# Optimization experiments

Hardware: AMD Instinct MI355X
Metric: run time of the kernel (lower is better)

## Reference

```python
import jax, jax.numpy as jnp
import numpy as np

B, N = 8, 2048          # clouds x points per cloud
M1, M2 = 1024, 256      # centroids after ratio 0.5, then 0.25
K = 64                  # max_num_neighbors
R1, R2 = 0.2, 0.4       # radii
CURV_K = 10             # knn for curvature
CURV_SCALAR = 10.0      # Net(curvature_scalar)
NEG = -1e30


def _sqdist(a, b):
    # squared pairwise distances [len(a), len(b)] without an [.,.,3] intermediate
    return jnp.sum(a * a, -1)[:, None] + jnp.sum(b * b, -1)[None, :] - 2.0 * (a @ b.T)


def _mlp3(x, Wa, ba, Wb, bb, Wc, bc):
    # torch_geometric MLP: Linear+ReLU hidden layers, plain last layer
    h = jax.nn.relu(x @ Wa + ba)
    h = jax.nn.relu(h @ Wb + bb)
    return h @ Wc + bc


def _curvature(pos):
    # per-point surface variation lambda_min / sum(lambda) over k-NN covariance
    d2 = _sqdist(pos, pos)                        # [N,N]
    _, idx = jax.lax.top_k(-d2, CURV_K)           # k nearest (incl. self)
    nbr = pos[idx]                                # [N,k,3]
    c = nbr - jnp.mean(nbr, 1, keepdims=True)
    cov = jnp.einsum('nki,nkj->nij', c, c) / CURV_K
    ev = jnp.linalg.eigvalsh(cov)                 # ascending
    return ev[:, 0] / (jnp.sum(ev, -1) + 1e-8)


def _fps_weighted(pos, curv, m):
    # farthest point sampling, min-distance score weighted by curvature
    w = 1.0 + CURV_SCALAR * curv
    d0 = jnp.sum((pos - pos[0]) ** 2, -1)
    def step(min_d2, _):
        i = jnp.argmax(min_d2 * w)
        nd = jnp.sum((pos - pos[i]) ** 2, -1)
        return jnp.minimum(min_d2, nd), i
    _, rest = jax.lax.scan(step, d0, None, length=m - 1)
    return jnp.concatenate([jnp.zeros((1,), rest.dtype), rest])


def _sa(x, pos, curv, m, r, params):
    # SAModule: weighted FPS -> radius grouping (cap K) -> PointNetConv (gather, MLP, max)
    idx = _fps_weighted(pos, curv, m)
    cpos = pos[idx]                               # [m,3]
    d2 = _sqdist(cpos, pos)                       # [m,N]
    score = jnp.where(d2 <= r * r, -d2, NEG)
    vals, nidx = jax.lax.top_k(score, K)          # up to K nearest within radius
    mask = vals > NEG * 0.5                       # [m,K]
    rel = pos[nidx] - cpos[:, None, :]            # [m,K,3]
    feats = rel if x is None else jnp.concatenate([x[nidx], rel], -1)
    msg = _mlp3(feats, *params)                   # [m,K,F]
    msg = jnp.where(mask[:, :, None], msg, NEG)
    out = jnp.max(msg, 1)                         # scatter-max aggregation
    out = jnp.where(jnp.any(mask, 1)[:, None], out, 0.0)  # empty groups -> 0
    return out, cpos, curv[idx]


def _forward(pos, W1a, b1a, W1b, b1b, W1c, b1c, W2a, b2a, W2b, b2b, W2c, b2c,
             W3a, b3a, W3b, b3b, W3c, b3c, Wh1, bh1, Wh2, bh2, Wh3, bh3):
    p1 = (W1a, b1a, W1b, b1b, W1c, b1c)
    p2 = (W2a, b2a, W2b, b2b, W2c, b2c)
    p3 = (W3a, b3a, W3b, b3b, W3c, b3c)
    def cloud(p):
        curv = _curvature(p)
        x1, pos1, c1 = _sa(None, p, curv, M1, R1, p1)
        x2, pos2, _ = _sa(x1, pos1, c1, M2, R2, p2)
        g = _mlp3(jnp.concatenate([x2, pos2], -1), *p3)   # [M2,1024]
        return jnp.max(g, 0)                              # global max pool
    gfeat = jax.vmap(cloud)(pos.reshape(B, N, 3))          # [B,1024]
    logits = _mlp3(gfeat, Wh1, bh1, Wh2, bh2, Wh3, bh3)    # dropout (eval) = id
    return jax.nn.log_softmax(logits, -1)


_LAYERS = [("W1a", "b1a", 3, 64), ("W1b", "b1b", 64, 64), ("W1c", "b1c", 64, 128),
           ("W2a", "b2a", 131, 128), ("W2b", "b2b", 128, 128), ("W2c", "b2c", 128, 256),
           ("W3a", "b3a", 259, 256), ("W3b", "b3b", 256, 512), ("W3c", "b3c", 512, 1024),
           ("Wh1", "bh1", 1024, 512), ("Wh2", "bh2", 512, 256), ("Wh3", "bh3", 256, 10)]


def setup_inputs() -> dict:
    key = jax.random.key(0)
    ks = iter(jax.random.split(key, 2 * len(_LAYERS) + 1))
    inp = {"pos": jax.random.uniform(next(ks), (B * N, 3), jnp.float32)}
    for wn, bn, fi, fo in _LAYERS:
        inp[wn] = jax.random.normal(next(ks), (fi, fo), jnp.float32) / np.sqrt(fi)
        inp[bn] = jnp.zeros((fo,), jnp.float32)
    return inp


def reference(pos, W1a, b1a, W1b, b1b, W1c, b1c, W2a, b2a, W2b, b2b, W2c, b2c,
              W3a, b3a, W3b, b3b, W3c, b3c, Wh1, bh1, Wh2, bh2, Wh3, bh3):
    return _forward(pos, W1a, b1a, W1b, b1b, W1c, b1c, W2a, b2a, W2b, b2b, W2c, b2c,
                    W3a, b3a, W3b, b3b, W3c, b3c, Wh1, bh1, Wh2, bh2, Wh3, bh3)
```

## Files before the change

### kernel.cpp

```cpp
#include <hip/hip_runtime.h>
#include <hip/hip_fp16.h>
#include <math.h>

#define TID threadIdx.x

typedef _Float16 h2vec __attribute__((ext_vector_type(2)));
typedef _Float16 f16x8 __attribute__((ext_vector_type(8)));
typedef float f32x4 __attribute__((ext_vector_type(4)));
typedef float f32x2v __attribute__((ext_vector_type(2)));

#if __has_builtin(__builtin_elementwise_fma)
#define EFMA(a, b, c) __builtin_elementwise_fma((a), (b), (c))
#else
static __device__ __forceinline__ f32x2v EFMA(f32x2v a, f32x2v b, f32x2v c) {
    f32x2v r;
    r.x = fmaf(a.x, b.x, c.x);
    r.y = fmaf(a.y, b.y, c.y);
    return r;
}
#endif

static __device__ __forceinline__ float fdot2(unsigned a, unsigned b, float c) {
    h2vec av, bv;
    __builtin_memcpy(&av, &a, 4);
    __builtin_memcpy(&bv, &b, 4);
    return __builtin_amdgcn_fdot2(av, bv, c, false);
}

static __device__ __forceinline__ unsigned packh2(float a, float b) {
    __half2 hh = __floats2half2_rn(a, b);
    unsigned u;
    __builtin_memcpy(&u, &hh, 4);
    return u;
}

static __device__ __forceinline__ unsigned encf(float f) {
    unsigned u = __float_as_uint(f);
    return (u >> 31) ? ~u : (u | 0x80000000u);
}
static __device__ __forceinline__ float decf(unsigned e) {
    unsigned u = (e >> 31) ? (e & 0x7fffffffu) : ~e;
    return __uint_as_float(u);
}

static __device__ __forceinline__ int wave_sum(int v) {
    v += __builtin_amdgcn_update_dpp(0, v, 0x111, 0xf, 0xf, true);
    v += __builtin_amdgcn_update_dpp(0, v, 0x112, 0xf, 0xf, true);
    v += __builtin_amdgcn_update_dpp(0, v, 0x114, 0xf, 0xf, true);
    v += __builtin_amdgcn_update_dpp(0, v, 0x118, 0xf, 0xf, true);
    v += __builtin_amdgcn_update_dpp(0, v, 0x142, 0xf, 0xf, true);
    v += __builtin_amdgcn_update_dpp(0, v, 0x143, 0xf, 0xf, true);
    return __builtin_amdgcn_readlane(v, 63);
}

template <int CTRL>
static __device__ __forceinline__ unsigned long long dpp_max_u64(unsigned long long k) {
    int lo = (int)(unsigned)(k & 0xffffffffULL);
    int hi = (int)(unsigned)(k >> 32);
    int lo2 = __builtin_amdgcn_update_dpp(0, lo, CTRL, 0xf, 0xf, true);
    int hi2 = __builtin_amdgcn_update_dpp(0, hi, CTRL, 0xf, 0xf, true);
    unsigned long long k2 = ((unsigned long long)(unsigned)hi2 << 32) | (unsigned)lo2;
    return k2 > k ? k2 : k;
}

static __device__ __forceinline__ void pack_slot(const float* __restrict__ W,
                                                 unsigned* __restrict__ out,
                                                 int K, int ncols, int t) {
    int lane = t & 63;
    int frag = t >> 6;
    int nct = ncols >> 4;
    int ks = frag / nct, ct = frag - ks * nct;
    int kbase = (ks << 5) + ((lane >> 4) << 3);
    int cc = (ct << 4) + (lane & 15);
    unsigned o[4];
#pragma unroll
    for (int i = 0; i < 4; ++i) {
        int k0 = kbase + 2 * i, k1 = kbase + 2 * i + 1;
        float f0 = (k0 < K) ? W[(size_t)k0 * ncols + cc] : 0.f;
        float f1 = (k1 < K) ? W[(size_t)k1 * ncols + cc] : 0.f;
        o[i] = packh2(f0, f1);
    }
    *(uint4*)&out[(size_t)t * 4] = make_uint4(o[0], o[1], o[2], o[3]);
}

__global__ __launch_bounds__(256) void curv_kernel(const float* __restrict__ pos,
                                                   float* __restrict__ curv) {
    __shared__ float4 sp[2048];
    __shared__ float smd[64][40];
    __shared__ int smi[64][40];
    int cloud = blockIdx.x >> 5;
    int base = cloud << 11;
    for (int j = TID; j < 2048; j += 256) {
        const float* p = pos + (size_t)(base + j) * 3;
        float x = p[0], y = p[1], z = p[2];
        sp[j] = make_float4(x, y, z, fmaf(x, x, fmaf(y, y, z * z)));
    }
    __syncthreads();
    int pt = TID >> 2;
    int sub = TID & 3;
    int li = ((blockIdx.x & 31) << 6) + pt;
    float4 pi = sp[li];
    float bd[10];
    int bi[10];
#pragma unroll
    for (int t = 0; t < 10; ++t) { bd[t] = 3.0e38f; bi[t] = 0; }
    int j0 = sub << 9;
    for (int jj = 0; jj < 512; ++jj) {
        int j = j0 + jj;
        float4 pj = sp[j];
        float dot = fmaf(pi.x, pj.x, fmaf(pi.y, pj.y, pi.z * pj.z));
        float d2 = pi.w + pj.w - 2.0f * dot;
        if (d2 < bd[9]) {
            bd[9] = d2; bi[9] = j;
#pragma unroll
            for (int t = 9; t > 0; --t) {
                if (bd[t] < bd[t - 1]) {
                    float td = bd[t]; bd[t] = bd[t - 1]; bd[t - 1] = td;
                    int ti = bi[t]; bi[t] = bi[t - 1]; bi[t - 1] = ti;
                }
            }
        }
    }
#pragma unroll
    for (int t = 0; t < 10; ++t) {
        smd[pt][sub * 10 + t] = bd[t];
        smi[pt][sub * 10 + t] = bi[t];
    }
    __syncthreads();
    float d0 = smd[pt][0], d1 = smd[pt][10], d2h = smd[pt][20], d3 = smd[pt][30];
    int i0 = smi[pt][0], i1 = smi[pt][10], i2 = smi[pt][20], i3 = smi[pt][30];
    int h0 = 0, h1 = 0, h2c = 0, h3 = 0;
    int mbi[10];
#pragma unroll
    for (int t = 0; t < 10; ++t) {
        bool a01 = (d1 < d0) || (d1 == d0 && i1 < i0);
        float dA = a01 ? d1 : d0; int iA = a01 ? i1 : i0;
        bool a23 = (d3 < d2h) || (d3 == d2h && i3 < i2);
        float dB = a23 ? d3 : d2h; int iB = a23 ? i3 : i2;
        bool ab = (dB < dA) || (dB == dA && iB < iA);
        mbi[t] = ab ? iB : iA;
        if (ab) {
            if (a23) { ++h3; d3 = (h3 < 10) ? smd[pt][30 + h3] : 3.0e38f;
                       i3 = (h3 < 10) ? smi[pt][30 + h3] : 0x7fffffff; }
            else     { ++h2c; d2h = (h2c < 10) ? smd[pt][20 + h2c] : 3.0e38f;
                       i2 = (h2c < 10) ? smi[pt][20 + h2c] : 0x7fffffff; }
        } else {
            if (a01) { ++h1; d1 = (h1 < 10) ? smd[pt][10 + h1] : 3.0e38f;
                       i1 = (h1 < 10) ? smi[pt][10 + h1] : 0x7fffffff; }
            else     { ++h0; d0 = (h0 < 10) ? smd[pt][h0] : 3.0e38f;
                       i0 = (h0 < 10) ? smi[pt][h0] : 0x7fffffff; }
        }
    }
    if (sub != 0) return;
    double sx = 0, sy = 0, sz = 0;
#pragma unroll
    for (int t = 0; t < 10; ++t) { float4 p = sp[mbi[t]]; sx += p.x; sy += p.y; sz += p.z; }
    double mx = sx / 10.0, my = sy / 10.0, mz = sz / 10.0;
    double cxx = 0, cxy = 0, cxz = 0, cyy = 0, cyz = 0, czz = 0;
#pragma unroll
    for (int t = 0; t < 10; ++t) {
        float4 p = sp[mbi[t]];
        double dx = p.x - mx, dy = p.y - my, dz = p.z - mz;
        cxx += dx * dx; cxy += dx * dy; cxz += dx * dz;
        cyy += dy * dy; cyz += dy * dz; czz += dz * dz;
    }
    cxx /= 10.0; cxy /= 10.0; cxz /= 10.0; cyy /= 10.0; cyz /= 10.0; czz /= 10.0;
    double q = (cxx + cyy + czz) / 3.0;
    double b00 = cxx - q, b11 = cyy - q, b22 = czz - q;
    double p2 = b00 * b00 + b11 * b11 + b22 * b22 +
                2.0 * (cxy * cxy + cxz * cxz + cyz * cyz);
    double lmin;
    if (p2 <= 0.0) {
        lmin = q;
    } else {
        double p = sqrt(p2 / 6.0);
        double inv = 1.0 / p;
        double c00 = b00 * inv, c01 = cxy * inv, c02 = cxz * inv;
        double c11 = b11 * inv, c12 = cyz * inv, c22 = b22 * inv;
        double detB = c00 * (c11 * c22 - c12 * c12)
                    - c01 * (c01 * c22 - c12 * c02)
                    + c02 * (c01 * c12 - c11 * c02);
        double r = 0.5 * detB;
        r = fmin(1.0, fmax(-1.0, r));
        double phi = acos(r) / 3.0;
        lmin = q + 2.0 * p * cos(phi + 2.0943951023931953);
    }
    double s3 = cxx + cyy + czz;
    curv[base + li] = (float)(lmin / (s3 + 1e-8));
}

template <int N, int M, int SLOTS>
static __device__ void fps_body(
    const float* __restrict__ srcpos, int stride, const float* __restrict__ srccurv,
    int cloud, float4* __restrict__ outPos, float* __restrict__ outCurv,
    float* __restrict__ outA, int ldA,
    float4* sp, int* sidx, unsigned long long* rec ) {
    constexpr int PAIRS = SLOTS / 2;
    const float* cp = srcpos + (size_t)cloud * N * stride;
    for (int j = TID; j < N; j += 256)
        sp[j] = make_float4(cp[j * stride], cp[j * stride + 1], cp[j * stride + 2], 0.f);
    if (TID == 0) sidx[0] = 0;
    __syncthreads();
    f32x2v px[PAIRS], py[PAIRS], pz[PAIRS], md[PAIRS], wvv[PAIRS];
#pragma unroll
    for (int s = 0; s < PAIRS; ++s) {
        int p0 = ((2 * s) << 8) + TID, p1 = ((2 * s + 1) << 8) + TID;
        float4 q0 = sp[p0], q1 = sp[p1];
        px[s].x = q0.x; px[s].y = q1.x;
        py[s].x = q0.y; py[s].y = q1.y;
        pz[s].x = q0.z; pz[s].y = q1.z;
        md[s].x = 3.0e38f; md[s].y = 3.0e38f;
        wvv[s].x = fmaf(10.0f, srccurv[cloud * N + p0], 1.0f);
        wvv[s].y = fmaf(10.0f, srccurv[cloud * N + p1], 1.0f);
    }
    int lane = TID & 63, w4 = TID >> 6;
    float4 c0 = sp[0];
    float cx = c0.x, cy = c0.y, cz = c0.z;
    for (int t = 1; t < M; ++t) {
        f32x2v cxv, cyv, czv;
        cxv.x = cx; cxv.y = cx; cyv.x = cy; cyv.y = cy; czv.x = cz; czv.y = cz;
        unsigned long long kk[PAIRS];
#pragma unroll
        for (int s = 0; s < PAIRS; ++s) {
            f32x2v dx = px[s] - cxv, dy = py[s] - cyv, dz = pz[s] - czv;
            f32x2v nd = EFMA(dx, dx, EFMA(dy, dy, dz * dz));
            f32x2v m2 = __builtin_elementwise_min(md[s], nd);
            md[s] = m2;
            f32x2v sc = m2 * wvv[s];
            unsigned long long k0 =
                ((unsigned long long)__float_as_uint(sc.x) << 32) |
                (unsigned)(2047 - (((2 * s) << 8) + TID));
            unsigned long long k1 =
                ((unsigned long long)__float_as_uint(sc.y) << 32) |
                (unsigned)(2047 - (((2 * s + 1) << 8) + TID));
            kk[s] = k0 > k1 ? k0 : k1;
        }
        unsigned long long k = kk[0];
#pragma unroll
        for (int s = 1; s < PAIRS; ++s) k = kk[s] > k ? kk[s] : k;
        k = dpp_max_u64<0x111>(k);
        k = dpp_max_u64<0x112>(k);
        k = dpp_max_u64<0x114>(k);
        k = dpp_max_u64<0x118>(k);
        k = dpp_max_u64<0x142>(k);
        k = dpp_max_u64<0x143>(k);
        int pbase = (t & 1) << 2;
        if (lane == 63) rec[pbase | w4] = k;
        __syncthreads();
        unsigned long long k0 = rec[pbase + 0];
        unsigned long long k1 = rec[pbase + 1];
        unsigned long long k2 = rec[pbase + 2];
        unsigned long long k3 = rec[pbase + 3];
        unsigned long long ka = k0 > k1 ? k0 : k1;
        unsigned long long kb = k2 > k3 ? k2 : k3;
        unsigned long long km = ka > kb ? ka : kb;
        int nbix = 2047 - (int)(unsigned)(km & 0xffffffffULL);
        if (TID == 0) sidx[t] = nbix;
        float4 cc = sp[nbix];
        cx = cc.x; cy = cc.y; cz = cc.z;
    }
    __syncthreads();
    for (int j = TID; j < M; j += 256) {
        int id = sidx[j];
        float4 qv = sp[id];
        outPos[cloud * M + j] = qv;
        if (outCurv) outCurv[cloud * M + j] = srccurv[cloud * N + id];
        if (outA) {
            float* a = outA + (size_t)(cloud * M + j) * ldA;
            a[256] = qv.x; a[257] = qv.y; a[258] = qv.z;
        }
    }
}

__global__ __launch_bounds__(256, 1) void fps1_pack_kernel(
    const float* __restrict__ pos, const float* __restrict__ curv,
    float4* __restrict__ pos1, float* __restrict__ curv1,
    const float* __restrict__ Wc, const float* __restrict__ Wa,
    const float* __restrict__ Wb, const float* __restrict__ W3a,
    const float* __restrict__ W3b, const float* __restrict__ W3c,
    unsigned* __restrict__ WcH, unsigned* __restrict__ WaH,
    unsigned* __restrict__ WbH, unsigned* __restrict__ W3aH,
    unsigned* __restrict__ W3bH, unsigned* __restrict__ W3cH,
    unsigned* __restrict__ gfeatE) {
    __shared__ float4 sp[2048];
    __shared__ int sidx[1024];
    __shared__ unsigned long long rec[8];
    if (blockIdx.x < 8) {
        fps_body<2048, 1024, 8>(pos, 3, curv, blockIdx.x, pos1, curv1, nullptr, 0,
                                sp, sidx, rec);
        return;
    }
    int b = blockIdx.x - 8;
    if (b == 0)
        for (int i = TID; i < 8192; i += 256) gfeatE[i] = 0u;
    if (b < 16)        pack_slot(Wc,  WcH,  128, 256,  b * 256 + TID);
    else if (b < 26)   pack_slot(Wa,  WaH,  131, 128,  (b - 16) * 256 + TID);
    else if (b < 34)   pack_slot(Wb,  WbH,  128, 128,  (b - 26) * 256 + TID);
    else if (b < 70)   pack_slot(W3a, W3aH, 259, 256,  (b - 34) * 256 + TID);
    else if (b < 134)  pack_slot(W3b, W3bH, 256, 512,  (b - 70) * 256 + TID);
    else               pack_slot(W3c, W3cH, 512, 1024, (b - 134) * 256 + TID);
}

static __device__ __forceinline__ int select_k64(const unsigned int* ck, const int* ci,
                                                 int c, int lane, int* cnt2, int* sel,
                                                 int* nbOut) {
    if (c <= 64) {
        *nbOut = c;
        return (lane < c) ? ci[lane] : 0;
    }
    unsigned int T = 0;
    for (int bit = 31; bit >= 0; --bit) {
        unsigned int mid = T | (1u << bit);
        int cl = 0;
        for (int q = lane; q < c; q += 64) cl += (ck[q] < mid) ? 1 : 0;
        if (wave_sum(cl) < 64) T = mid;
    }
    int cl = 0;
    for (int q = lane; q < c; q += 64) cl += (ck[q] < T) ? 1 : 0;
    int need = 64 - wave_sum(cl);
    int TI = 0;
    for (int bit = 11; bit >= 0; --bit) {
        int mid = TI | (1 << bit);
        int ce = 0;
        for (int q = lane; q < c; q += 64) ce += (ck[q] == T && ci[q] < mid) ? 1 : 0;
        if (wave_sum(ce) < need) TI = mid;
    }
    for (int q = lane; q < c; q += 64) {
        unsigned int kq = ck[q];
        int iq = ci[q];
        if (kq < T || (kq == T && iq <= TI)) sel[atomicAdd(cnt2, 1)] = iq;
    }
    *nbOut = 64;
    return sel[lane];
}

union U1 {
    struct {
        float4 sp[2048];
        unsigned ck[4][256];
        int ci[4][256];
        int sel[4][64];
        int cnt[4], cnt2[4];
    } p;
    unsigned h2s[4][2048];
};

static __device__ void conv1_body(
    int bid, U1& u,
    const float* __restrict__ pos, const float4* __restrict__ pos1,
    const float* __restrict__ W1, const float* __restrict__ B1,
    const float* __restrict__ W2, const float* __restrict__ B2,
    const float* __restrict__ W3, const float* __restrict__ B3,
    float* __restrict__ x1) {
    __shared__ int nbs[4];
    int cloud = bid >> 8;
    int w4 = TID >> 6, lane = TID & 63;
    int centb = (bid & 255) << 2;
    int g = (cloud << 10) + centb + w4;
    int base = cloud << 11;
    for (int j = TID; j < 2048; j += 256) {
        const float* p = pos + (size_t)(base + j) * 3;
        u.p.sp[j] = make_float4(p[0], p[1], p[2], 0.f);
    }
    if (lane == 0) { u.p.cnt[w4] = 0; u.p.cnt2[w4] = 0; }
    __syncthreads();
    float4 cq = pos1[g];
    double cx = cq.x, cy = cq.y, cz = cq.z;
    for (int s = 0; s < 32; ++s) {
        int j = (s << 6) + lane;
        float4 pj = u.p.sp[j];
        double dx = (double)pj.x - cx, dy = (double)pj.y - cy, dz = (double)pj.z - cz;
        double d2 = dx * dx + dy * dy + dz * dz;
        if (d2 <= 0.2 * 0.2) {
            int p = atomicAdd(&u.p.cnt[w4], 1);
            if (p < 256) { u.p.ck[w4][p] = __float_as_uint((float)d2); u.p.ci[w4][p] = j; }
        }
    }
    __syncthreads();
    int c = min(u.p.cnt[w4], 256);
    int nb;
    int idxn = select_k64(u.p.ck[w4], u.p.ci[w4], c, lane, &u.p.cnt2[w4],
                          u.p.sel[w4], &nb);
    if (lane == 0) nbs[w4] = nb;
    float4 pn = u.p.sp[idxn];
    float rx = pn.x - cq.x, ry = pn.y - cq.y, rz = pn.z - cq.z;
    float h1[64];
#pragma unroll
    for (int cc2 = 0; cc2 < 64; ++cc2) {
        float v = fmaf(rx, W1[cc2], fmaf(ry, W1[64 + cc2], fmaf(rz, W1[128 + cc2], B1[cc2])));
        h1[cc2] = fmaxf(v, 0.f);
    }
    float h2[64];
#pragma unroll
    for (int cc2 = 0; cc2 < 64; ++cc2) h2[cc2] = B2[cc2];
#pragma unroll
    for (int i = 0; i < 64; ++i) {
        float hv = h1[i];
        const float* wr = W2 + i * 64;
#pragma unroll
        for (int cc2 = 0; cc2 < 64; ++cc2) h2[cc2] = fmaf(hv, wr[cc2], h2[cc2]);
    }
#pragma unroll
    for (int cc2 = 0; cc2 < 64; ++cc2) h2[cc2] = fmaxf(h2[cc2], 0.f);
    __syncthreads();
    {
        unsigned* hrow = &u.h2s[w4][lane << 5];
        int sw = (lane & 7) << 2;
#pragma unroll
        for (int q = 0; q < 8; ++q) {
            unsigned tmp[4];
#pragma unroll
            for (int k2 = 0; k2 < 4; ++k2) {
                int j = (q << 2) + k2;
                tmp[k2] = packh2(h2[2 * j], h2[2 * j + 1]);
            }
            *(uint4*)&hrow[(q << 2) ^ sw] = make_uint4(tmp[0], tmp[1], tmp[2], tmp[3]);
        }
    }
    __syncthreads();
    int ch = ((w4 & 1) << 6) + lane;
    int cbase = (w4 >> 1) << 1;
    unsigned w2[32];
#pragma unroll
    for (int p = 0; p < 32; ++p)
        w2[p] = packh2(W3[(2 * p) * 128 + ch], W3[(2 * p + 1) * 128 + ch]);
    float bv = B3[ch];
#pragma unroll 1
    for (int ci2 = 0; ci2 < 2; ++ci2) {
        int cc = cbase + ci2;
        int nbc = nbs[cc];
        float m = -1e30f;
        for (int n = 0; n < nbc; ++n) {
            const unsigned* hr = &u.h2s[cc][n << 5];
            int sw2 = (n & 7) << 2;
            float a0 = 0.f, a1 = 0.f, a2 = 0.f, a3 = 0.f;
#pragma unroll
            for (int q = 0; q < 8; ++q) {
                uint4 hv = *(const uint4*)&hr[(q << 2) ^ sw2];
                a0 = fdot2(hv.x, w2[(q << 2) + 0], a0);
                a1 = fdot2(hv.y, w2[(q << 2) + 1], a1);
                a2 = fdot2(hv.z, w2[(q << 2) + 2], a2);
                a3 = fdot2(hv.w, w2[(q << 2) + 3], a3);
            }
            m = fmaxf(m, bv + (a0 + a1) + (a2 + a3));
        }
        x1[(size_t)((cloud << 10) + centb + cc) * 128 + ch] = m;
    }
}

union UM {
    U1 c;
    struct {
        float4 sp[1024];
        unsigned long long rec[8];
        int sidx[256];
    } f;
};

__global__ __launch_bounds__(256, 2) void fps2_conv1_kernel(
    const float* __restrict__ pos, const float4* __restrict__ pos1,
    const float* __restrict__ curv1, float4* __restrict__ pos2,
    float* __restrict__ Abuf,
    const float* __restrict__ W1, const float* __restrict__ B1,
    const float* __restrict__ W2, const float* __restrict__ B2,
    const float* __restrict__ W3, const float* __restrict__ B3,
    float* __restrict__ x1) {
    __shared__ UM u;
    if (blockIdx.x < 8) {
        fps_body<1024, 256, 4>((const float*)pos1, 4, curv1, blockIdx.x, pos2,
                               nullptr, Abuf, 260, u.f.sp, u.f.sidx, u.f.rec);
    } else {
        conv1_body(blockIdx.x - 8, u.c, pos, pos1, W1, B1, W2, B2, W3, B3, x1);
    }
}

union U2 {
    struct {
        float4 sp[1024];
        unsigned ck[4][512];
        int ci[4][512];
        int sel[4][64];
        int cnt[4], cnt2[4];
    } p;
    unsigned xs[4][5376];
};

__global__ __launch_bounds__(256, 1) void conv2_kernel(
    const float4* __restrict__ pos1, const float4* __restrict__ pos2,
    const float* __restrict__ x1,
    const unsigned* __restrict__ WaH, const float* __restrict__ Ba,
    const unsigned* __restrict__ WbH, const float* __restrict__ Bb,
    const unsigned* __restrict__ WcH, const float* __restrict__ Bc,
    float* __restrict__ Aout) {
    __shared__ U2 u;
    __shared__ unsigned h1s[4][4352];
    __shared__ int nbs[4];
    int cloud = blockIdx.x >> 6;
    int w4 = TID >> 6, lane = TID & 63;
    int centb = (blockIdx.x & 63) << 2;
    int g = (cloud << 8) + centb + w4;
    int quad = lane >> 4, l15 = lane & 15;
    for (int j = TID; j < 1024; j += 256) u.p.sp[j] = pos1[(cloud << 10) + j];
    if (lane == 0) { u.p.cnt[w4] = 0; u.p.cnt2[w4] = 0; }
    __syncthreads();
    float4 cq = pos2[g];
    double cx = cq.x, cy = cq.y, cz = cq.z;
    for (int s = 0; s < 16; ++s) {
        int j = (s << 6) + lane;
        float4 pj = u.p.sp[j];
        double dx = (double)pj.x - cx, dy = (double)pj.y - cy, dz = (double)pj.z - cz;
        double d2 = dx * dx + dy * dy + dz * dz;
        if (d2 <= 0.4 * 0.4) {
            int p = atomicAdd(&u.p.cnt[w4], 1);
            if (p < 512) { u.p.ck[w4][p] = __float_as_uint((float)d2); u.p.ci[w4][p] = j; }
        }
    }
    __syncthreads();
    int c = min(u.p.cnt[w4], 512);
    int nb;
    int idxn = select_k64(u.p.ck[w4], u.p.ci[w4], c, lane, &u.p.cnt2[w4],
                          u.p.sel[w4], &nb);
    if (lane == 0) nbs[w4] = nb;
    float4 pn = u.p.sp[idxn];
    float rx = pn.x - cq.x, ry = pn.y - cq.y, rz = pn.z - cq.z;
    __syncthreads();
    {
        const float4* xr = (const float4*)(x1 + (size_t)((cloud << 10) + idxn) * 128);
        unsigned* row = &u.xs[w4][lane * 84];
#pragma unroll
        for (int q = 0; q < 16; ++q) {
            float4 a = xr[q * 2], b = xr[q * 2 + 1];
            *(uint4*)&row[q << 2] = make_uint4(packh2(a.x, a.y), packh2(a.z, a.w),
                                               packh2(b.x, b.y), packh2(b.z, b.w));
        }
        *(uint4*)&row[64] = make_uint4(packh2(rx, ry), packh2(rz, 0.f), 0u, 0u);
        *(uint4*)&row[68] = make_uint4(0u, 0u, 0u, 0u);
        *(uint4*)&row[72] = make_uint4(0u, 0u, 0u, 0u);
        *(uint4*)&row[76] = make_uint4(0u, 0u, 0u, 0u);
    }
    float ba8[8];
#pragma unroll
    for (int ct = 0; ct < 8; ++ct) ba8[ct] = Ba[(ct << 4) + l15];
#pragma unroll 1
    for (int ct = 0; ct < 8; ++ct) {
        f16x8 bfrag[5];
#pragma unroll
        for (int ks = 0; ks < 5; ++ks) {
            uint4 bv = *(const uint4*)&WaH[(size_t)((((ks << 3) | ct) << 6) | lane) << 2];
            __builtin_memcpy(&bfrag[ks], &bv, 16);
        }
#pragma unroll
        for (int rt = 0; rt < 4; ++rt) {
            f32x4 acc = {0.f, 0.f, 0.f, 0.f};
#pragma unroll
            for (int ks = 0; ks < 5; ++ks) {
                f16x8 af;
                uint4 av = *(const uint4*)&u.xs[w4][((rt << 4) + l15) * 84 +
                                                    (((ks << 2) + quad) << 2)];
                __builtin_memcpy(&af, &av, 16);
                acc = __builtin_amdgcn_mfma_f32_16x16x32_f16(af, bfrag[ks], acc, 0, 0, 0);
            }
#pragma unroll
            for (int r = 0; r < 4; ++r) {
                float v = fmaxf(acc[r] + ba8[ct], 0.f);
                float vp = __shfl_xor(v, 1, 64);
                if (!(l15 & 1)) {
                    int rowi = (rt << 4) + (quad << 2) + r;
                    h1s[w4][rowi * 68 + (ct << 3) + (l15 >> 1)] = packh2(v, vp);
                }
            }
        }
    }
    unsigned* h2w = &u.xs[w4][0];
#pragma unroll
    for (int ct = 0; ct < 8; ++ct) ba8[ct] = Bb[(ct << 4) + l15];
#pragma unroll 1
    for (int ct = 0; ct < 8; ++ct) {
        f16x8 bfrag[4];
#pragma unroll
        for (int ks = 0; ks < 4; ++ks) {
            uint4 bv = *(const uint4*)&WbH[(size_t)((((ks << 3) | ct) << 6) | lane) << 2];
            __builtin_memcpy(&bfrag[ks], &bv, 16);
        }
#pragma unroll
        for (int rt = 0; rt < 4; ++rt) {
            f32x4 acc = {0.f, 0.f, 0.f, 0.f};
#pragma unroll
            for (int ks = 0; ks < 4; ++ks) {
                f16x8 af;
                uint4 av = *(const uint4*)&h1s[w4][((rt << 4) + l15) * 68 +
                                                   (((ks << 2) + quad) << 2)];
                __builtin_memcpy(&af, &av, 16);
                acc = __builtin_amdgcn_mfma_f32_16x16x32_f16(af, bfrag[ks], acc, 0, 0, 0);
            }
#pragma unroll
            for (int r = 0; r < 4; ++r) {
                float v = fmaxf(acc[r] + ba8[ct], 0.f);
                float vp = __shfl_xor(v, 1, 64);
                if (!(l15 & 1)) {
                    int rowi = (rt << 4) + (quad << 2) + r;
                    int d = (ct << 3) + (l15 >> 1);
                    int ch = d >> 2, din = d & 3;
                    h2w[(rowi << 6) + ((ch ^ (rowi & 15)) << 2) + din] = packh2(v, vp);
                }
            }
        }
    }
    __syncthreads();
    int ctb = w4 << 2;
    f16x8 cfrag[4][4];
#pragma unroll
    for (int ct = 0; ct < 4; ++ct)
#pragma unroll
        for (int ks = 0; ks < 4; ++ks) {
            uint4 bv = *(const uint4*)&WcH[(size_t)((((ks << 4) | (ctb + ct)) << 6) | lane) << 2];
            __builtin_memcpy(&cfrag[ct][ks], &bv, 16);
        }
#pragma unroll 1
    for (int cent = 0; cent < 4; ++cent) {
        const unsigned* h2r = &u.xs[cent][0];
        int nbc = nbs[cent];
        float runM[4][4];
#pragma unroll
        for (int ct = 0; ct < 4; ++ct)
#pragma unroll
            for (int r = 0; r < 4; ++r) runM[ct][r] = -1e30f;
#pragma unroll
        for (int rt = 0; rt < 4; ++rt) {
            int nl = (rt << 4) + l15;
            f16x8 afrag[4];
#pragma unroll
            for (int ks = 0; ks < 4; ++ks) {
                int cp = ((ks << 2) | quad) ^ l15;
                uint4 av = *(const uint4*)&h2r[(nl << 6) + (cp << 2)];
                __builtin_memcpy(&afrag[ks], &av, 16);
            }
#pragma unroll
            for (int ct = 0; ct < 4; ++ct) {
                f32x4 acc = {0.f, 0.f, 0.f, 0.f};
#pragma unroll
                for (int ks = 0; ks < 4; ++ks)
                    acc = __builtin_amdgcn_mfma_f32_16x16x32_f16(afrag[ks], cfrag[ct][ks],
                                                                 acc, 0, 0, 0);
                int nb0 = (rt << 4) + (quad << 2);
#pragma unroll
                for (int r = 0; r < 4; ++r) {
                    float v = (nb0 + r < nbc) ? acc[r] : -1e30f;
                    runM[ct][r] = fmaxf(runM[ct][r], v);
                }
            }
        }
#pragma unroll
        for (int ct = 0; ct < 4; ++ct) {
            float m = fmaxf(fmaxf(runM[ct][0], runM[ct][1]),
                            fmaxf(runM[ct][2], runM[ct][3]));
            m = fmaxf(m, __shfl_xor(m, 16, 64));
            m = fmaxf(m, __shfl_xor(m, 32, 64));
            if (lane < 16) {
                int cc = ((ctb + ct) << 4) | l15;
                Aout[(size_t)((cloud << 8) + centb + cent) * 260 + cc] = m + Bc[cc];
            }
        }
    }
}

__global__ __launch_bounds__(256) void gemm_mfma2(
    const float* __restrict__ A, int lda, const unsigned* __restrict__ Bp, int nct,
    const float* __restrict__ bias, float* __restrict__ C, int ldc, int K,
    int relu, unsigned* __restrict__ gmax) {
    int w = (blockIdx.x << 2) + (TID >> 6);
    int ncg = nct >> 3;
    int rs = w / ncg, cg = w - rs * ncg;
    int r0 = rs << 4, ct0 = cg << 3;
    int lane = TID & 63, quad = lane >> 4, l15 = lane & 15;
    f32x4 acc[8];
#pragma unroll
    for (int ct = 0; ct < 8; ++ct) acc[ct] = (f32x4){0.f, 0.f, 0.f, 0.f};
    const float* ar = A + (size_t)(r0 + l15) * lda;
    int nks = (K + 31) >> 5;
    for (int ks = 0; ks < nks; ++ks) {
        int kb = (ks << 5) + (quad << 3);
        f16x8 af;
        if (kb + 8 <= K) {
            float4 a0 = *(const float4*)(ar + kb);
            float4 a1 = *(const float4*)(ar + kb + 4);
            uint4 av = make_uint4(packh2(a0.x, a0.y), packh2(a0.z, a0.w),
                                  packh2(a1.x, a1.y), packh2(a1.z, a1.w));
            __builtin_memcpy(&af, &av, 16);
        } else {
            float f[8];
#pragma unroll
            for (int j = 0; j < 8; ++j) f[j] = (kb + j < K) ? ar[kb + j] : 0.f;
            uint4 av = make_uint4(packh2(f[0], f[1]), packh2(f[2], f[3]),
                                  packh2(f[4], f[5]), packh2(f[6], f[7]));
            __builtin_memcpy(&af, &av, 16);
        }
#pragma unroll
        for (int ct = 0; ct < 8; ++ct) {
            uint4 bv = *(const uint4*)&Bp[(size_t)(((ks * nct + ct0 + ct) << 6) | lane) << 2];
            f16x8 bf;
            __builtin_memcpy(&bf, &bv, 16);
            acc[ct] = __builtin_amdgcn_mfma_f32_16x16x32_f16(af, bf, acc[ct], 0, 0, 0);
        }
    }
    if (!gmax) {
#pragma unroll
        for (int ct = 0; ct < 8; ++ct) {
            int col = ((ct0 + ct) << 4) + l15;
            float bb = bias[col];
#pragma unroll
            for (int r = 0; r < 4; ++r) {
                int row = r0 + (quad << 2) + r;
                float v = acc[ct][r] + bb;
                if (relu) v = fmaxf(v, 0.f);
                C[(size_t)row * ldc + col] = v;
            }
        }
    } else {
        int cloud = r0 >> 8;
#pragma unroll
        for (int ct = 0; ct < 8; ++ct) {
            int col = ((ct0 + ct) << 4) + l15;
            float bb = bias[col];
            float m = fmaxf(fmaxf(acc[ct][0], acc[ct][1]),
                            fmaxf(acc[ct][2], acc[ct][3])) + bb;
            m = fmaxf(m, __shfl_xor(m, 16, 64));
            m = fmaxf(m, __shfl_xor(m, 32, 64));
            if (quad == 0) atomicMax(&gmax[(cloud << 10) + col], encf(m));
        }
    }
}

__global__ __launch_bounds__(256) void head_kernel(
    const unsigned* __restrict__ gfeatE,
    const float* __restrict__ Wh1, const float* __restrict__ bh1,
    const float* __restrict__ Wh2, const float* __restrict__ bh2,
    const float* __restrict__ Wh3, const float* __restrict__ bh3,
    float* __restrict__ out) {
    __shared__ float gg[1024];
    __shared__ float s1[512];
    __shared__ float s2[256];
    __shared__ float lg[10];
    int cloud = blockIdx.x;
    for (int i = TID; i < 1024; i += 256) gg[i] = decf(gfeatE[(cloud << 10) + i]);
    __syncthreads();
    for (int cc = TID; cc < 512; cc += 256) {
        float v = bh1[cc];
        for (int i = 0; i < 1024; ++i) v = fmaf(gg[i], Wh1[i * 512 + cc], v);
        s1[cc] = fmaxf(v, 0.f);
    }
    __syncthreads();
    for (int cc = TID; cc < 256; cc += 256) {
        float v = bh2[cc];
        for (int i = 0; i < 512; ++i) v = fmaf(s1[i], Wh2[i * 256 + cc], v);
        s2[cc] = fmaxf(v, 0.f);
    }
    __syncthreads();
    if (TID < 10) {
        float v = bh3[TID];
        for (int i = 0; i < 256; ++i) v = fmaf(s2[i], Wh3[i * 10 + TID], v);
        lg[TID] = v;
    }
    __syncthreads();
    if (TID == 0) {
        float mx = lg[0];
        for (int i = 1; i < 10; ++i) mx = fmaxf(mx, lg[i]);
        float s = 0.f;
        for (int i = 0; i < 10; ++i) s += expf(lg[i] - mx);
        float lse = mx + logf(s);
        for (int i = 0; i < 10; ++i) out[cloud * 10 + i] = lg[i] - lse;
    }
}

extern "C" void kernel_launch(void* const* d_in, const int* in_sizes, int n_in,
                              void* d_out, int out_size, void* d_ws, size_t ws_size,
                              hipStream_t stream) {
    (void)in_sizes; (void)n_in; (void)out_size; (void)ws_size;
    const float* pos = (const float*)d_in[0];
    const float* W1a = (const float*)d_in[1];  const float* b1a = (const float*)d_in[2];
    const float* W1b = (const float*)d_in[3];  const float* b1b = (const float*)d_in[4];
    const float* W1c = (const float*)d_in[5];  const float* b1c = (const float*)d_in[6];
    const float* W2a = (const float*)d_in[7];  const float* b2a = (const float*)d_in[8];
    const float* W2b = (const float*)d_in[9];  const float* b2b = (const float*)d_in[10];
    const float* W2c = (const float*)d_in[11]; const float* b2c = (const float*)d_in[12];
    const float* W3a = (const float*)d_in[13]; const float* b3a = (const float*)d_in[14];
    const float* W3b = (const float*)d_in[15]; const float* b3b = (const float*)d_in[16];
    const float* W3c = (const float*)d_in[17]; const float* b3c = (const float*)d_in[18];
    const float* Wh1 = (const float*)d_in[19]; const float* bh1 = (const float*)d_in[20];
    const float* Wh2 = (const float*)d_in[21]; const float* bh2 = (const float*)d_in[22];
    const float* Wh3 = (const float*)d_in[23]; const float* bh3 = (const float*)d_in[24];

    char* ws = (char*)d_ws;
    float*    curv   = (float*)(ws + 0);
    float4*   pos1   = (float4*)(ws + 98304);
    float*    curv1  = (float*)(ws + 229376);
    float4*   pos2   = (float4*)(ws + 270336);
    unsigned* gfeatE = (unsigned*)(ws + 303104);
    unsigned* WcH    = (unsigned*)(ws + 335872);
    unsigned* WaH    = (unsigned*)(ws + 401408);
    unsigned* WbH    = (unsigned*)(ws + 442368);
    float*    x1     = (float*)(ws + 524288);
    float*    Abuf   = (float*)(ws + 4718592);
    float*    h1g    = (float*)(ws + 6848512);
    unsigned* W3aH   = (unsigned*)(ws + 8945664);
    unsigned* W3bH   = (unsigned*)(ws + 9093120);
    unsigned* W3cH   = (unsigned*)(ws + 9355264);
    float*    h2g    = x1;

    curv_kernel<<<256, 256, 0, stream>>>(pos, curv);
    fps1_pack_kernel<<<398, 256, 0, stream>>>(pos, curv, pos1, curv1,
                                              W2c, W2a, W2b, W3a, W3b, W3c,
                                              WcH, WaH, WbH, W3aH, W3bH, W3cH,
                                              gfeatE);
    fps2_conv1_kernel<<<2056, 256, 0, stream>>>(pos, pos1, curv1, pos2, Abuf,
                                                W1a, b1a, W1b, b1b, W1c, b1c, x1);
    conv2_kernel<<<512, 256, 0, stream>>>(pos1, pos2, x1, WaH, b2a, WbH, b2b, WcH, b2c,
                                          Abuf);
    gemm_mfma2<<<64, 256, 0, stream>>>(Abuf, 260, W3aH, 16, b3a, h1g, 256,
                                       259, 1, nullptr);
    gemm_mfma2<<<128, 256, 0, stream>>>(h1g, 256, W3bH, 32, b3b, h2g, 512,
                                        256, 1, nullptr);
    gemm_mfma2<<<256, 256, 0, stream>>>(h2g, 512, W3cH, 64, b3c, nullptr, 0,
                                        512, 0, gfeatE);
    head_kernel<<<8, 256, 0, stream>>>(gfeatE, Wh1, bh1, Wh2, bh2, Wh3, bh3,
                                       (float*)d_out);
}
```

Before: 1.197 ms.

## Use ballot compaction and register-resident k-selection in conv1, raise occupancy

Replaces the shared-memory atomic counter used for radius-neighbor compaction with wave ballot and prefix popcount, which removes a block-wide barrier. Adds a register-based top-64 selection that skips selection when there are 64 or fewer candidates, and removes excess candidates with DPP max reductions when there are few extra. The second MLP layer is computed in two 32-channel halves to cut register pressure, and launch bounds are raised to three blocks per CU. Lower register budgets risk spills, and the fps blocks in the same kernel share the new launch bound.

After: 1.167 ms. 1.03x faster.

```diff
diff --git a/kernel.cpp b/kernel.cpp
--- a/kernel.cpp
+++ b/kernel.cpp
@@ -334,13 +334,98 @@
     return sel[lane];
 }
 
+static __device__ __forceinline__ int select_k64_fast(
+    const unsigned* __restrict__ ck, const int* __restrict__ ci,
+    int c, int lane, int* sel, int* nbOut) {
+    if (c <= 64) {
+        *nbOut = c;
+        return (lane < c) ? ci[lane] : 0;
+    }
+    unsigned long long kq[4];
+    bool act[4];
+#pragma unroll
+    for (int q = 0; q < 4; ++q) {
+        int idx = (q << 6) + lane;
+        bool v = idx < c;
+        act[q] = v;
+        kq[q] = v ? (((unsigned long long)ck[idx] << 32) | (unsigned)ci[idx]) : 0ULL;
+    }
+    int excess = c - 64;
+    if (excess <= 24) {
+        for (int r = 0; r < excess; ++r) {
+            unsigned long long k = 0;
+#pragma unroll
+            for (int q = 0; q < 4; ++q) {
+                unsigned long long kc = act[q] ? kq[q] : 0ULL;
+                k = kc > k ? kc : k;
+            }
+            k = dpp_max_u64<0x111>(k);
+            k = dpp_max_u64<0x112>(k);
+            k = dpp_max_u64<0x114>(k);
+            k = dpp_max_u64<0x118>(k);
+            k = dpp_max_u64<0x142>(k);
+            k = dpp_max_u64<0x143>(k);
+            unsigned klo = (unsigned)__builtin_amdgcn_readlane(
+                (int)(unsigned)(k & 0xffffffffULL), 63);
+            unsigned khi = (unsigned)__builtin_amdgcn_readlane(
+                (int)(unsigned)(k >> 32), 63);
+            unsigned long long km = ((unsigned long long)khi << 32) | klo;
+#pragma unroll
+            for (int q = 0; q < 4; ++q)
+                if (act[q] && kq[q] == km) act[q] = false;
+        }
+    } else {
+        unsigned T = 0;
+        for (int bit = 31; bit >= 0; --bit) {
+            unsigned mid = T | (1u << bit);
+            int cl = 0;
+#pragma unroll
+            for (int q = 0; q < 4; ++q)
+                cl += (act[q] && (unsigned)(kq[q] >> 32) < mid) ? 1 : 0;
+            if (wave_sum(cl) < 64) T = mid;
+        }
+        int cl = 0;
+#pragma unroll
+        for (int q = 0; q < 4; ++q)
+            cl += (act[q] && (unsigned)(kq[q] >> 32) < T) ? 1 : 0;
+        int need = 64 - wave_sum(cl);
+        int TI = 0;
+        for (int bit = 11; bit >= 0; --bit) {
+            int mid = TI | (1 << bit);
+            int ce = 0;
+#pragma unroll
+            for (int q = 0; q < 4; ++q)
+                ce += (act[q] && (unsigned)(kq[q] >> 32) == T &&
+                       (int)(unsigned)(kq[q] & 0xffffffffULL) < mid) ? 1 : 0;
+            if (wave_sum(ce) < need) TI = mid;
+        }
+#pragma unroll
+        for (int q = 0; q < 4; ++q) {
+            unsigned hi = (unsigned)(kq[q] >> 32);
+            int lo = (int)(unsigned)(kq[q] & 0xffffffffULL);
+            act[q] = act[q] && (hi < T || (hi == T && lo <= TI));
+        }
+    }
+    int base = 0;
+#pragma unroll
+    for (int q = 0; q < 4; ++q) {
+        unsigned long long m = __ballot(act[q]);
+        if (act[q]) {
+            int off = __popcll(m & ((1ULL << lane) - 1));
+            sel[base + off] = (int)(unsigned)(kq[q] & 0xffffffffULL);
+        }
+        base += __popcll(m);
+    }
+    *nbOut = 64;
+    return sel[lane];
+}
+
 union U1 {
     struct {
         float4 sp[2048];
         unsigned ck[4][256];
         int ci[4][256];
         int sel[4][64];
-        int cnt[4], cnt2[4];
     } p;
     unsigned h2s[4][2048];
 };
@@ -362,59 +447,66 @@
         const float* p = pos + (size_t)(base + j) * 3;
         u.p.sp[j] = make_float4(p[0], p[1], p[2], 0.f);
     }
-    if (lane == 0) { u.p.cnt[w4] = 0; u.p.cnt2[w4] = 0; }
     __syncthreads();
     float4 cq = pos1[g];
     double cx = cq.x, cy = cq.y, cz = cq.z;
+    int cnt = 0;
     for (int s = 0; s < 32; ++s) {
         int j = (s << 6) + lane;
         float4 pj = u.p.sp[j];
         double dx = (double)pj.x - cx, dy = (double)pj.y - cy, dz = (double)pj.z - cz;
         double d2 = dx * dx + dy * dy + dz * dz;
-        if (d2 <= 0.2 * 0.2) {
-            int p = atomicAdd(&u.p.cnt[w4], 1);
-            if (p < 256) { u.p.ck[w4][p] = __float_as_uint((float)d2); u.p.ci[w4][p] = j; }
-        }
-    }
-    __syncthreads();
-    int c = min(u.p.cnt[w4], 256);
+        bool in = (d2 <= 0.2 * 0.2);
+        unsigned long long m = __ballot(in);
+        if (in) {
+            int p = cnt + __popcll(m & ((1ULL << lane) - 1));
+            if (p < 256) {
+                u.p.ck[w4][p] = __float_as_uint((float)d2);
+                u.p.ci[w4][p] = j;
+            }
+        }
+        cnt += __popcll(m);
+    }
+    int c = min(cnt, 256);
     int nb;
-    int idxn = select_k64(u.p.ck[w4], u.p.ci[w4], c, lane, &u.p.cnt2[w4],
-                          u.p.sel[w4], &nb);
+    int idxn = select_k64_fast(u.p.ck[w4], u.p.ci[w4], c, lane, u.p.sel[w4], &nb);
     if (lane == 0) nbs[w4] = nb;
     float4 pn = u.p.sp[idxn];
     float rx = pn.x - cq.x, ry = pn.y - cq.y, rz = pn.z - cq.z;
+    __syncthreads();
     float h1[64];
 #pragma unroll
     for (int cc2 = 0; cc2 < 64; ++cc2) {
         float v = fmaf(rx, W1[cc2], fmaf(ry, W1[64 + cc2], fmaf(rz, W1[128 + cc2], B1[cc2])));
         h1[cc2] = fmaxf(v, 0.f);
     }
-    float h2[64];
-#pragma unroll
-    for (int cc2 = 0; cc2 < 64; ++cc2) h2[cc2] = B2[cc2];
-#pragma unroll
-    for (int i = 0; i < 64; ++i) {
-        float hv = h1[i];
-        const float* wr = W2 + i * 64;
-#pragma unroll
-        for (int cc2 = 0; cc2 < 64; ++cc2) h2[cc2] = fmaf(hv, wr[cc2], h2[cc2]);
-    }
-#pragma unroll
-    for (int cc2 = 0; cc2 < 64; ++cc2) h2[cc2] = fmaxf(h2[cc2], 0.f);
-    __syncthreads();
-    {
+#pragma unroll 1
+    for (int half = 0; half < 2; ++half) {
+        int c0 = half << 5;
+        float h2[32];
+#pragma unroll
+        for (int t = 0; t < 32; ++t) h2[t] = B2[c0 + t];
+#pragma unroll
+        for (int i = 0; i < 64; ++i) {
+            float hv = h1[i];
+            const float* wr = W2 + i * 64 + c0;
+#pragma unroll
+            for (int t = 0; t < 32; ++t) h2[t] = fmaf(hv, wr[t], h2[t]);
+        }
+#pragma unroll
+        for (int t = 0; t < 32; ++t) h2[t] = fmaxf(h2[t], 0.f);
         unsigned* hrow = &u.h2s[w4][lane << 5];
         int sw = (lane & 7) << 2;
 #pragma unroll
-        for (int q = 0; q < 8; ++q) {
+        for (int q = 0; q < 4; ++q) {
             unsigned tmp[4];
 #pragma unroll
             for (int k2 = 0; k2 < 4; ++k2) {
-                int j = (q << 2) + k2;
-                tmp[k2] = packh2(h2[2 * j], h2[2 * j + 1]);
-            }
-            *(uint4*)&hrow[(q << 2) ^ sw] = make_uint4(tmp[0], tmp[1], tmp[2], tmp[3]);
+                int jp = (q << 2) + k2;
+                tmp[k2] = packh2(h2[2 * jp], h2[2 * jp + 1]);
+            }
+            int qg = (half << 2) + q;
+            *(uint4*)&hrow[(qg << 2) ^ sw] = make_uint4(tmp[0], tmp[1], tmp[2], tmp[3]);
         }
     }
     __syncthreads();
@@ -457,7 +549,7 @@
     } f;
 };
 
-__global__ __launch_bounds__(256, 2) void fps2_conv1_kernel(
+__global__ __launch_bounds__(256, 3) void fps2_conv1_kernel(
     const float* __restrict__ pos, const float4* __restrict__ pos1,
     const float* __restrict__ curv1, float4* __restrict__ pos2,
     float* __restrict__ Abuf,
```
